# Performance work log

Hardware: AMD Instinct MI355X
Metric: run time of the kernel (lower is better)

The kernel has to match this reference:

```python
import jax, jax.numpy as jnp
import numpy as np

B, N, T, F_IN, H, E = 64, 325, 24, 64, 64, 2600
NEG_SLOPE = 0.2


def setup_inputs() -> dict:
    key = jax.random.key(0)
    k1, k2, k3, k4, k5 = jax.random.split(key, 5)
    x = jax.random.normal(k1, (B, N, T, F_IN), dtype=jnp.float32)
    edge_index = jax.random.randint(k2, (2, E), 0, N, dtype=jnp.int32)
    scale = 1.0 / np.sqrt(F_IN)
    W = jax.random.normal(k3, (H, F_IN), dtype=jnp.float32) * scale
    att_src = jax.random.normal(k4, (H,), dtype=jnp.float32) * scale
    att_dst = jax.random.normal(k5, (H,), dtype=jnp.float32) * scale
    bias = jnp.zeros((H,), dtype=jnp.float32)
    return {"x": x, "edge_index": edge_index, "W": W,
            "att_src": att_src, "att_dst": att_dst, "bias": bias}


def reference(x, edge_index, W, att_src, att_dst, bias):
    b, n, t, nf = x.shape
    # Fold the B*T graph replicas into one leading axis: [G, N, F]
    xg = x.transpose(0, 2, 1, 3).reshape(b * t, n, nf)
    h = jnp.einsum('gnf,hf->gnh', xg, W)  # linear transform [G, N, H]
    a_s = h @ att_src  # [G, N] per-node source attention logit
    a_d = h @ att_dst  # [G, N] per-node dest attention logit
    src, dst = edge_index[0], edge_index[1]
    # Per-edge raw score (gather), LeakyReLU as in GATConv: [G, E]
    e = jax.nn.leaky_relu(a_s[:, src] + a_d[:, dst], negative_slope=NEG_SLOPE)

    def per_graph(e_g, h_g):
        # segment softmax over edges grouped by destination node
        m = jax.ops.segment_max(e_g, dst, num_segments=n)
        ex = jnp.exp(e_g - m[dst])
        den = jax.ops.segment_sum(ex, dst, num_segments=n)
        alpha = ex / den[dst]  # [E]
        msg = alpha[:, None] * h_g[src]  # [E, H]
        return jax.ops.segment_sum(msg, dst, num_segments=n)  # [N, H]

    out = jax.vmap(per_graph)(e, h) + bias  # [G, N, H]
    out = jax.nn.gelu(out, approximate=False)
    # Faithful to source: view(B,T,N,H) then raw reshape(B,N,T,H) (row-major reinterpret)
    return out.reshape(b, n, t, -1)
```

## Files before the change

### kernel.cpp

```cpp
#include <hip/hip_runtime.h>
#include <hip/hip_bf16.h>

#define B_  64
#define N_  325
#define T_  24
#define F_  64
#define H_  64
#define E_  2600
#define G_  (B_ * T_)
#define BLK 512
#define GRID4 768
#define HS  68

using half2_t = __attribute__((ext_vector_type(2))) _Float16;
using half8_t = __attribute__((ext_vector_type(8))) _Float16;
using f32x4   = __attribute__((ext_vector_type(4))) float;

__global__ __launch_bounds__(512) void k_off_prep(
    const int* __restrict__ ei, int* __restrict__ csr_off,
    unsigned short* __restrict__ perm) {
  __shared__ int cnt[N_];
  const int tid = threadIdx.x;
  for (int i = tid; i < N_; i += BLK) cnt[i] = 0;
  __syncthreads();
  for (int e = tid; e < E_; e += BLK) atomicAdd(&cnt[ei[E_ + e]], 1);
  __syncthreads();
  if (tid <= N_) {
    int off = 0;
    for (int m = 0; m < N_; ++m) off += (m < tid) ? cnt[m] : 0;
    csr_off[tid] = off;
  }
  if (tid < N_) {
    const int c = cnt[tid];
    int r = 0;
    for (int m = 0; m < N_; ++m) {
      const int cm = cnt[m];
      r += (cm > c || (cm == c && m < tid)) ? 1 : 0;
    }
    perm[r] = (unsigned short)tid;
  }
}

__global__ __launch_bounds__(64) void k_scatter(const int* __restrict__ ei,
                                                const int* __restrict__ csr_off,
                                                unsigned short* __restrict__ csr_src) {
  __shared__ int dsts[E_];
  const int tid = threadIdx.x;
  for (int i = tid; i < E_; i += 64) dsts[i] = ei[E_ + i];
  __syncthreads();
  const int e = blockIdx.x * 64 + tid;
  if (e >= E_) return;
  const int myd = dsts[e];
  int rank = 0;
#pragma unroll 4
  for (int k = 0; k < e; ++k) rank += (dsts[k] == myd) ? 1 : 0;
  csr_src[csr_off[myd] + rank] = (unsigned short)ei[e];
}

__device__ __forceinline__ float f16lo(unsigned u) {
  half2_t h = __builtin_bit_cast(half2_t, u); return (float)h[0];
}
__device__ __forceinline__ float f16hi(unsigned u) {
  half2_t h = __builtin_bit_cast(half2_t, u); return (float)h[1];
}
__device__ __forceinline__ unsigned short f16b(float f) {
  _Float16 h = (_Float16)f; return __builtin_bit_cast(unsigned short, h);
}
__device__ __forceinline__ half2_t pkrtz(float a, float b) {
  return __builtin_bit_cast(half2_t, __builtin_amdgcn_cvt_pkrtz(a, b));
}
__device__ __forceinline__ half8_t pk8(float4 a, float4 b) {
  half2_t p0 = pkrtz(a.x, a.y);
  half2_t p1 = pkrtz(a.z, a.w);
  half2_t p2 = pkrtz(b.x, b.y);
  half2_t p3 = pkrtz(b.z, b.w);
  half8_t r;
  r[0] = p0[0]; r[1] = p0[1]; r[2] = p1[0]; r[3] = p1[1];
  r[4] = p2[0]; r[5] = p2[1]; r[6] = p3[0]; r[7] = p3[1];
  return r;
}

__device__ __forceinline__ float gelu_f(float v) {
  float t = v * (1.5957691216f + 0.0713550903f * (v * v));
  t = fminf(t, 80.0f);
  float e = __expf(t);
  return v * e * __builtin_amdgcn_rcpf(e + 1.0f);
}

__global__ __launch_bounds__(512, 6) void k_gat6(
    const float* __restrict__ x, const int* __restrict__ csr_off_g,
    const unsigned short* __restrict__ csr_src_g,
    const unsigned short* __restrict__ perm_g, const float* __restrict__ W,
    const float* __restrict__ att_src, const float* __restrict__ att_dst,
    const float* __restrict__ bias, float* __restrict__ out) {
  __shared__ _Float16 h_s[N_][HS];
  __shared__ unsigned short src_s[E_];
  __shared__ unsigned asad_s[N_];
  __shared__ float att_s[2 * H_];
  __shared__ unsigned short coff_s[N_ + 1];
  __shared__ unsigned short perm_s[N_];

  const int tid  = threadIdx.x;
  const int lane = tid & 63;
  const int wv   = tid >> 6;
  const int l15  = lane & 15;
  const int l4   = lane >> 4;

  for (int i = tid; i < E_; i += BLK) src_s[i] = csr_src_g[i];
  for (int i = tid; i <= N_; i += BLK) coff_s[i] = csr_off_g[i];
  for (int i = tid; i < N_; i += BLK) perm_s[i] = perm_g[i];
  if (tid < H_) { att_s[tid] = att_src[tid]; att_s[H_ + tid] = att_dst[tid]; }

  half8_t bf[2][4];
#pragma unroll
  for (int ct = 0; ct < 4; ++ct)
#pragma unroll
    for (int k0 = 0; k0 < 2; ++k0) {
      const float* p = W + (size_t)(ct * 16 + l15) * F_ + k0 * 32 + l4 * 8;
      bf[k0][ct] = pk8(*(const float4*)p, *(const float4*)(p + 4));
    }

  const int l16v = tid & 15;
  const int qw   = tid >> 4;
  const float4 bias4 = *(const float4*)(bias + 4 * l16v);

  for (int gi = 0; gi < 2; ++gi) {
    const int g  = blockIdx.x + gi * GRID4;
    const int bb = g / T_;
    const int tt = g % T_;
    if (gi) __syncthreads();

    const float* xg = x + ((size_t)bb * N_ * T_ + tt) * F_;
#pragma unroll
    for (int ti = 0; ti < 3; ++ti) {
      const int t = wv + ti * 8;
      int tc = t > 20 ? 20 : t;
      int rr = tc * 16 + l15; if (rr > N_ - 1) rr = N_ - 1;
      const float* xr = xg + (size_t)rr * (T_ * F_) + l4 * 8;
      const float4 u0 = *(const float4*)xr;
      const float4 u1 = *(const float4*)(xr + 4);
      const float4 u2 = *(const float4*)(xr + 32);
      const float4 u3 = *(const float4*)(xr + 36);
      if (t < 21) {
        const int r0 = t * 16;
        const half8_t a0 = pk8(u0, u1);
        const half8_t a1 = pk8(u2, u3);
        const bool full = (r0 + 16 <= N_);
#pragma unroll
        for (int ct = 0; ct < 4; ++ct) {
          f32x4 acc = {0.f, 0.f, 0.f, 0.f};
          acc = __builtin_amdgcn_mfma_f32_16x16x32_f16(a0, bf[0][ct], acc, 0, 0, 0);
          acc = __builtin_amdgcn_mfma_f32_16x16x32_f16(a1, bf[1][ct], acc, 0, 0, 0);
          const int col = ct * 16 + l15;
#pragma unroll
          for (int j = 0; j < 4; ++j) {
            const int row = r0 + l4 * 4 + j;
            if (full || row < N_) h_s[row][col] = (_Float16)acc[j];
          }
        }
      }
    }
    __syncthreads();

    for (int j = tid; j < 2 * N_; j += BLK) {
      const int n   = j >> 1;
      const int sel = j & 1;
      const unsigned* hr = (const unsigned*)&h_s[n][0];
      const float2* av = (const float2*)(att_s + sel * H_);
      float acc = 0.f;
#pragma unroll
      for (int i = 0; i < 32; ++i) {
        const unsigned hp = hr[i];
        const float2 a2 = av[i];
        acc += f16lo(hp) * a2.x + f16hi(hp) * a2.y;
      }
      ((unsigned short*)asad_s)[n * 2 + sel] = f16b(acc);
    }
    __syncthreads();

    for (int idx = qw; idx < N_; idx += 32) {
      const int n   = perm_s[idx];
      const int beg = coff_s[n], end = coff_s[n + 1];
      const float adn = f16hi(asad_s[n]);
      half2_t a01 = {(_Float16)0.f, (_Float16)0.f};
      half2_t a23 = {(_Float16)0.f, (_Float16)0.f};
      float den = 0.f;
      for (int p = beg; p < end; ++p) {
        const int s = src_s[p];
        float e = f16lo(asad_s[s]) + adn;
        e = fmaxf(e, 0.2f * e);
        const float ex =
            __builtin_amdgcn_exp2f(__builtin_fmaf(e, 1.44269504f, -7.21347520f));
        den += ex;
        const half2_t al2 = pkrtz(ex, ex);
        const uint2 hv = *(const uint2*)&h_s[s][4 * l16v];
        a01 = al2 * __builtin_bit_cast(half2_t, hv.x) + a01;
        a23 = al2 * __builtin_bit_cast(half2_t, hv.y) + a23;
      }
      const float inv = (end > beg) ? __builtin_amdgcn_rcpf(den) : 0.0f;
      const float v0 = gelu_f((float)a01[0] * inv + bias4.x);
      const float v1 = gelu_f((float)a01[1] * inv + bias4.y);
      const float v2 = gelu_f((float)a23[0] * inv + bias4.z);
      const float v3 = gelu_f((float)a23[1] * inv + bias4.w);
      *(float4*)&out[((size_t)g * N_ + n) * H_ + 4 * l16v] =
          make_float4(v0, v1, v2, v3);
    }
  }
}

extern "C" void kernel_launch(void* const* d_in, const int* in_sizes, int n_in,
                              void* d_out, int out_size, void* d_ws, size_t ws_size,
                              hipStream_t stream) {
  (void)in_sizes; (void)n_in; (void)out_size; (void)ws_size;
  const float* x       = (const float*)d_in[0];
  const int*   ei      = (const int*)d_in[1];
  const float* W       = (const float*)d_in[2];
  const float* att_src = (const float*)d_in[3];
  const float* att_dst = (const float*)d_in[4];
  const float* bias    = (const float*)d_in[5];
  float* out = (float*)d_out;

  char* ws = (char*)d_ws;
  int*            csr_off = (int*)(ws + 0);
  unsigned short* csr_src = (unsigned short*)(ws + 4096);
  unsigned short* perm    = (unsigned short*)(ws + 16384);

  k_off_prep<<<1, BLK, 0, stream>>>(ei, csr_off, perm);
  k_scatter<<<(E_ + 63) / 64, 64, 0, stream>>>(ei, csr_off, csr_src);
  k_gat6<<<GRID4, BLK, 0, stream>>>(x, csr_off, csr_src, perm, W, att_src, att_dst,
                                    bias, out);
}
```

Measured before the change: 127.4 us.

## Precompute per-edge exp weights once per graph and software-pipeline aggregation loop

Adds a per-edge pass that computes the LeakyReLU/exp attention weight once per graph and packs it with the source index into shared memory. Previously the 16 lanes handling a destination node all recomputed it. The aggregation loop now prefetches packed edge entries and h rows several edges ahead to hide LDS latency. The grid drops to 512 blocks with 3 graphs per block and occupancy hint 4, which trades more per-block reuse for an extra barrier and pass and a larger edge buffer in LDS.

```diff
diff --git a/kernel.cpp b/kernel.cpp
--- a/kernel.cpp
+++ b/kernel.cpp
@@ -9,7 +9,7 @@
 #define E_  2600
 #define G_  (B_ * T_)
 #define BLK 512
-#define GRID4 768
+#define GRID3 512
 #define HS  68
 
 using half2_t = __attribute__((ext_vector_type(2))) _Float16;
@@ -43,7 +43,8 @@
 
 __global__ __launch_bounds__(64) void k_scatter(const int* __restrict__ ei,
                                                 const int* __restrict__ csr_off,
-                                                unsigned short* __restrict__ csr_src) {
+                                                unsigned short* __restrict__ csr_src,
+                                                unsigned short* __restrict__ edst) {
   __shared__ int dsts[E_];
   const int tid = threadIdx.x;
   for (int i = tid; i < E_; i += 64) dsts[i] = ei[E_ + i];
@@ -54,7 +55,9 @@
   int rank = 0;
 #pragma unroll 4
   for (int k = 0; k < e; ++k) rank += (dsts[k] == myd) ? 1 : 0;
-  csr_src[csr_off[myd] + rank] = (unsigned short)ei[e];
+  const int pos = csr_off[myd] + rank;
+  csr_src[pos] = (unsigned short)ei[e];
+  edst[pos]    = (unsigned short)myd;
 }
 
 __device__ __forceinline__ float f16lo(unsigned u) {
@@ -87,14 +90,15 @@
   return v * e * __builtin_amdgcn_rcpf(e + 1.0f);
 }
 
-__global__ __launch_bounds__(512, 6) void k_gat6(
+__global__ __launch_bounds__(512, 4) void k_gat7(
     const float* __restrict__ x, const int* __restrict__ csr_off_g,
     const unsigned short* __restrict__ csr_src_g,
-    const unsigned short* __restrict__ perm_g, const float* __restrict__ W,
+    const unsigned short* __restrict__ perm_g,
+    const unsigned short* __restrict__ edst_g, const float* __restrict__ W,
     const float* __restrict__ att_src, const float* __restrict__ att_dst,
     const float* __restrict__ bias, float* __restrict__ out) {
   __shared__ _Float16 h_s[N_][HS];
-  __shared__ unsigned short src_s[E_];
+  __shared__ unsigned pack_s[E_];
   __shared__ unsigned asad_s[N_];
   __shared__ float att_s[2 * H_];
   __shared__ unsigned short coff_s[N_ + 1];
@@ -106,7 +110,7 @@
   const int l15  = lane & 15;
   const int l4   = lane >> 4;
 
-  for (int i = tid; i < E_; i += BLK) src_s[i] = csr_src_g[i];
+  for (int i = tid; i < E_; i += BLK) pack_s[i] = (unsigned)csr_src_g[i];
   for (int i = tid; i <= N_; i += BLK) coff_s[i] = csr_off_g[i];
   for (int i = tid; i < N_; i += BLK) perm_s[i] = perm_g[i];
   if (tid < H_) { att_s[tid] = att_src[tid]; att_s[H_ + tid] = att_dst[tid]; }
@@ -124,8 +128,8 @@
   const int qw   = tid >> 4;
   const float4 bias4 = *(const float4*)(bias + 4 * l16v);
 
-  for (int gi = 0; gi < 2; ++gi) {
-    const int g  = blockIdx.x + gi * GRID4;
+  for (int gi = 0; gi < 3; ++gi) {
+    const int g  = blockIdx.x + (gi << 9);
     const int bb = g / T_;
     const int tt = g % T_;
     if (gi) __syncthreads();
@@ -178,24 +182,44 @@
     }
     __syncthreads();
 
+    for (int p = tid; p < E_; p += BLK) {
+      const unsigned sp = pack_s[p] & 0xffffu;
+      const int dp = edst_g[p];
+      float e = f16lo(asad_s[sp]) + f16hi(asad_s[dp]);
+      e = fmaxf(e, 0.2f * e);
+      const float ex =
+          __builtin_amdgcn_exp2f(__builtin_fmaf(e, 1.44269504f, -7.21347520f));
+      pack_s[p] = sp | ((unsigned)f16b(ex) << 16);
+    }
+    __syncthreads();
+
     for (int idx = qw; idx < N_; idx += 32) {
       const int n   = perm_s[idx];
       const int beg = coff_s[n], end = coff_s[n + 1];
-      const float adn = f16hi(asad_s[n]);
+      float den = 0.f;
       half2_t a01 = {(_Float16)0.f, (_Float16)0.f};
       half2_t a23 = {(_Float16)0.f, (_Float16)0.f};
-      float den = 0.f;
-      for (int p = beg; p < end; ++p) {
-        const int s = src_s[p];
-        float e = f16lo(asad_s[s]) + adn;
-        e = fmaxf(e, 0.2f * e);
-        const float ex =
-            __builtin_amdgcn_exp2f(__builtin_fmaf(e, 1.44269504f, -7.21347520f));
-        den += ex;
-        const half2_t al2 = pkrtz(ex, ex);
-        const uint2 hv = *(const uint2*)&h_s[s][4 * l16v];
-        a01 = al2 * __builtin_bit_cast(half2_t, hv.x) + a01;
-        a23 = al2 * __builtin_bit_cast(half2_t, hv.y) + a23;
+      if (beg < end) {
+        const int e1 = end - 1;
+        const int i1 = (beg + 1 > e1) ? e1 : beg + 1;
+        const int i2 = (beg + 2 > e1) ? e1 : beg + 2;
+        unsigned eu0 = pack_s[beg];
+        unsigned eu1 = pack_s[i1];
+        unsigned eu2 = pack_s[i2];
+        uint2 hv0 = *(const uint2*)&h_s[eu0 & 0xffffu][4 * l16v];
+        uint2 hv1 = *(const uint2*)&h_s[eu1 & 0xffffu][4 * l16v];
+        for (int p = beg; p < end; ++p) {
+          den += f16hi(eu0);
+          const unsigned au = eu0 >> 16;
+          const half2_t al = __builtin_bit_cast(half2_t, au | (au << 16));
+          a01 = al * __builtin_bit_cast(half2_t, hv0.x) + a01;
+          a23 = al * __builtin_bit_cast(half2_t, hv0.y) + a23;
+          const int i3 = (p + 3 > e1) ? e1 : p + 3;
+          eu0 = eu1; hv0 = hv1;
+          eu1 = eu2;
+          eu2 = pack_s[i3];
+          hv1 = *(const uint2*)&h_s[eu1 & 0xffffu][4 * l16v];
+        }
       }
       const float inv = (end > beg) ? __builtin_amdgcn_rcpf(den) : 0.0f;
       const float v0 = gelu_f((float)a01[0] * inv + bias4.x);
@@ -224,9 +248,10 @@
   int*            csr_off = (int*)(ws + 0);
   unsigned short* csr_src = (unsigned short*)(ws + 4096);
   unsigned short* perm    = (unsigned short*)(ws + 16384);
+  unsigned short* edst    = (unsigned short*)(ws + 20480);
 
   k_off_prep<<<1, BLK, 0, stream>>>(ei, csr_off, perm);
-  k_scatter<<<(E_ + 63) / 64, 64, 0, stream>>>(ei, csr_off, csr_src);
-  k_gat6<<<GRID4, BLK, 0, stream>>>(x, csr_off, csr_src, perm, W, att_src, att_dst,
-                                    bias, out);
-}
+  k_scatter<<<(E_ + 63) / 64, 64, 0, stream>>>(ei, csr_off, csr_src, edst);
+  k_gat7<<<GRID3, BLK, 0, stream>>>(x, csr_off, csr_src, perm, edst, W, att_src,
+                                    att_dst, bias, out);
+}
```

Measured after the change: 129.3 us. No clear change (+1.5%).
